# Kernel tuning notes

Hardware: AMD Instinct MI355X
Metric: run time of the kernel (lower is better)

The kernel has to match this reference:

```python
import jax, jax.numpy as jnp
import numpy as np
from jax import lax

DN = ('NCHW', 'OIHW', 'NCHW')

def _conv(x, w, b):
    y = lax.conv_general_dilated(x, w, (1, 1), 'SAME', dimension_numbers=DN)
    return y + b[None, :, None, None]

def setup_inputs() -> dict:
    key = jax.random.key(0)
    ks = jax.random.split(key, 11)
    B, C, H, W = 8, 16, 64, 64
    hid, K = 128, 8192
    s = 0.02
    return {
        'x': jax.random.normal(ks[0], (B, C, H, W), jnp.float32),
        # encoder: Conv2d(C->hid,3x3), GELU, Conv2d(hid->hid,3x3), GELU
        'ew1': jax.random.normal(ks[1], (hid, C, 3, 3), jnp.float32) * s,
        'eb1': jnp.zeros((hid,), jnp.float32),
        'ew2': jax.random.normal(ks[2], (hid, hid, 3, 3), jnp.float32) * s,
        'eb2': jnp.zeros((hid,), jnp.float32),
        # codebook: Embedding(K, hid), init normal std=0.02
        'embed': jax.random.normal(ks[3], (K, hid), jnp.float32) * s,
        # decoder: Conv2d(hid->hid,3x3), GELU, Conv2d(hid->C,1x1), sigmoid
        'dw1': jax.random.normal(ks[4], (hid, hid, 3, 3), jnp.float32) * s,
        'db1': jnp.zeros((hid,), jnp.float32),
        'dw2': jax.random.normal(ks[5], (C, hid, 1, 1), jnp.float32) * s,
        'db2': jnp.zeros((C,), jnp.float32),
    }

def reference(x, ew1, eb1, ew2, eb2, embed, dw1, db1, dw2, db2):
    # --- encoder ---
    h = jax.nn.gelu(_conv(x, ew1, eb1), approximate=False)
    h = jax.nn.gelu(_conv(h, ew2, eb2), approximate=False)  # [B, D, H, W]
    B, D, H, W = h.shape
    flat = jnp.transpose(h, (0, 2, 3, 1)).reshape(B * H * W, D)  # [N, D]
    # --- VQ: pairwise sq-dist + argmin (no_grad in original) ---
    flat_ng = lax.stop_gradient(flat)
    d2 = (jnp.sum(flat_ng * flat_ng, axis=1, keepdims=True)
          - 2.0 * flat_ng @ embed.T
          + jnp.sum(embed * embed, axis=1)[None, :])  # [N, K]
    idx = jnp.argmin(d2, axis=1)  # [N]
    z = idx.reshape(B, H, W)
    q = embed[idx].reshape(B, H, W, D)  # gather
    # --- decoder ---
    qc = jnp.transpose(q, (0, 3, 1, 2))  # NCHW
    y = jax.nn.gelu(_conv(qc, dw1, db1), approximate=False)
    x_hat = jax.nn.sigmoid(_conv(y, dw2, db2))  # [B, C, H, W]
    return x_hat
```

## Files before the change

### kernel.cpp

```cpp
#include <hip/hip_runtime.h>

constexpr int B_ = 8, H_ = 64, W_ = 64, C0 = 16, D_ = 128, K_ = 8192;
constexpr int N_ = B_ * H_ * W_;

typedef __attribute__((ext_vector_type(8))) short short8;
typedef __attribute__((ext_vector_type(4))) float f32x4;

__device__ __forceinline__ float gelu_f(float x) {
    return 0.5f * x * (1.0f + erff(x * 0.70710678118654752440f));
}

__device__ __forceinline__ unsigned short f2bf(float f) {
    unsigned u = __float_as_uint(f);
    u += 0x7fffu + ((u >> 16) & 1u);
    return (unsigned short)(u >> 16);
}

__device__ __forceinline__ void gload_lds16(const void* g, void* l) {
    __builtin_amdgcn_global_load_lds(
        (const __attribute__((address_space(1))) unsigned int*)g,
        (__attribute__((address_space(3))) unsigned int*)l, 16, 0, 0);
}

__global__ __launch_bounds__(256) void prep_kernel(
    const float* __restrict__ x, const float* __restrict__ ew1,
    const float* __restrict__ ew2, const float* __restrict__ dw1,
    const float* __restrict__ embed, unsigned short* __restrict__ xtbf,
    unsigned short* __restrict__ wtbf2, unsigned short* __restrict__ wtbf3,
    float* __restrict__ e2n, unsigned short* __restrict__ embbf,
    unsigned short* __restrict__ wtb1b,
    unsigned long long* __restrict__ partial,
    unsigned short* __restrict__ embq) {
    __shared__ float xt[16][66];
    int blk = blockIdx.x;
    int tid = threadIdx.x;
    if (blk < 512) {
        int b = blk >> 6, h = blk & 63;
        int c = tid >> 4, w4 = tid & 15;
        float4 v = ((const float4*)x)[(b * 16 + c) * 1024 + h * 16 + w4];
        xt[c][w4 * 4 + 0] = v.x;
        xt[c][w4 * 4 + 1] = v.y;
        xt[c][w4 * 4 + 2] = v.z;
        xt[c][w4 * 4 + 3] = v.w;
        __syncthreads();
        int w = tid >> 2, cg = (tid & 3) * 4;
        ushort4 o;
        o.x = f2bf(xt[cg + 0][w]);
        o.y = f2bf(xt[cg + 1][w]);
        o.z = f2bf(xt[cg + 2][w]);
        o.w = f2bf(xt[cg + 3][w]);
        *(ushort4*)(xtbf + (((b * 64 + h) * 64 + w) << 4) + cg) = o;
    } else if (blk < 1664) {
        const float* src = (blk < 1088) ? ew2 : dw1;
        unsigned short* dst = (blk < 1088) ? wtbf2 : wtbf3;
        int i = (blk - ((blk < 1088) ? 512 : 1088)) * 256 + tid;
        int ci = i & 127, co = (i >> 7) & 127, t = i >> 14;
        dst[i] = f2bf(src[(co * 128 + ci) * 9 + t]);
    } else if (blk < 1696) {
        int k = (blk - 1664) * 256 + tid;
        const float4* e4 = (const float4*)(embed + (size_t)k * 128);
        float s = 0.0f;
#pragma unroll 8
        for (int i = 0; i < 32; ++i) {
            float4 v = e4[i];
            s += v.x * v.x + v.y * v.y + v.z * v.z + v.w * v.w;
        }
        e2n[k] = -0.5f * s;
    } else if (blk < 2720) {
        int i = (blk - 1696) * 256 + tid;
        float4 v = ((const float4*)embed)[i];
        uint2 o;
        o.x = (unsigned)f2bf(v.x) | ((unsigned)f2bf(v.y) << 16);
        o.y = (unsigned)f2bf(v.z) | ((unsigned)f2bf(v.w) << 16);
        ((uint2*)embbf)[i] = o;
    } else if (blk < 2800) {
        int i = (blk - 2720) * 256 + tid;
        int co = i / 160, kk = i % 160;
        float v = 0.0f;
        if (kk < 144) {
            int t = kk >> 4, ci = kk & 15;
            v = ew1[(co * 16 + ci) * 9 + t];
        }
        wtb1b[i] = f2bf(v);
    } else if (blk < 2928) {
        int i = (blk - 2800) * 256 + tid;
        partial[i] = 0ULL;
    } else {
        int s = (blk - 2928) * 256 + tid;
        int T = s >> 10;
        int rem = s & 1023;
        int kk = rem >> 8, nsp = (rem >> 6) & 3, q = (rem >> 4) & 3,
            r = rem & 15;
        int code = T * 64 + nsp * 16 + r;
        int d0 = kk * 32 + q * 8;
        const float* ep = embed + (size_t)code * 128 + d0;
        unsigned short* op = embq + (size_t)s * 8;
#pragma unroll
        for (int e = 0; e < 8; ++e) op[e] = f2bf(ep[e]);
    }
}

__global__ __launch_bounds__(256, 2) void conv1_mfma_kernel(
    const unsigned short* __restrict__ xtbf,
    const unsigned short* __restrict__ wtb1b,
    const float* __restrict__ bias,
    unsigned short* __restrict__ out) {
    constexpr int LDA = 168;
    __shared__ __align__(16) unsigned short As[64 * LDA];
    int tid = threadIdx.x;
    int wv = tid >> 6, lane = tid & 63;
    int r = lane & 15, q = lane >> 4;
    int h0 = blockIdx.x & 63, b = blockIdx.x >> 6;

    short8 bf1[5][2];
#pragma unroll
    for (int k = 0; k < 5; ++k)
#pragma unroll
        for (int ns = 0; ns < 2; ++ns)
            bf1[k][ns] = *(const short8*)(wtb1b + (wv * 32 + ns * 16 + r) * 160 +
                                          k * 32 + q * 8);

#pragma unroll
    for (int j = 0; j < 5; ++j) {
        int s = tid + j * 256;
        if (s < 1152) {
            int px = s / 18, rem = s % 18;
            int t = rem >> 1, half = rem & 1;
            int hh = h0 + t / 3 - 1, ww = px + t % 3 - 1;
            float4 v = make_float4(0.f, 0.f, 0.f, 0.f);
            if ((unsigned)hh < 64u && (unsigned)ww < 64u)
                v = *(const float4*)(xtbf + (((b * 64 + hh) * 64 + ww) << 4) +
                                     half * 8);
            *(float4*)(As + px * LDA + t * 16 + half * 8) = v;
        } else {
            int z = s - 1152;
            int px = z >> 1, half = z & 1;
            *(float4*)(As + px * LDA + 144 + half * 8) =
                make_float4(0.f, 0.f, 0.f, 0.f);
        }
    }
    __syncthreads();

    f32x4 acc[4][2];
#pragma unroll
    for (int ms = 0; ms < 4; ++ms)
#pragma unroll
        for (int ns = 0; ns < 2; ++ns) acc[ms][ns] = (f32x4){0.f, 0.f, 0.f, 0.f};

#pragma unroll
    for (int k = 0; k < 5; ++k) {
        short8 af[4];
#pragma unroll
        for (int ms = 0; ms < 4; ++ms)
            af[ms] = *(const short8*)(As + (ms * 16 + r) * LDA + k * 32 + q * 8);
#pragma unroll
        for (int ms = 0; ms < 4; ++ms)
#pragma unroll
            for (int ns = 0; ns < 2; ++ns)
                acc[ms][ns] = __builtin_amdgcn_mfma_f32_16x16x32_bf16(
                    af[ms], bf1[k][ns], acc[ms][ns], 0, 0, 0);
    }

#pragma unroll
    for (int ns = 0; ns < 2; ++ns) {
        int co = wv * 32 + ns * 16 + r;
        float bv = bias[co];
#pragma unroll
        for (int ms = 0; ms < 4; ++ms)
#pragma unroll
            for (int rg = 0; rg < 4; ++rg) {
                int px = ms * 16 + q * 4 + rg;
                int pix = (b * 64 + h0) * 64 + px;
                out[(size_t)pix * 128 + co] = f2bf(gelu_f(acc[ms][ns][rg] + bv));
            }
    }
}

template <bool OUT_BF16, bool GATHER, bool FUSE>
__global__ __launch_bounds__(256, 2) void conv3x3_mfma_kernel(
    const unsigned short* __restrict__ in,
    const unsigned long long* __restrict__ gidx,
    const unsigned short* __restrict__ wtb,
    const float* __restrict__ bias,
    const float* __restrict__ w2,
    const float* __restrict__ b2,
    void* __restrict__ out_) {
    constexpr int LDC = 136;
    __shared__ __align__(16) unsigned short As[3 * 66 * LDC];
    __shared__ __align__(16) float ws2[FUSE ? 2048 : 4];
    int tid = threadIdx.x;
    int wv = tid >> 6, lane = tid & 63;
    int r = lane & 15, q = lane >> 4;
    int h0 = blockIdx.x & 63, b = blockIdx.x >> 6;

    constexpr int NJ = FUSE ? 15 : 13;
    for (int j = 0; j < NJ; ++j) {
        int s = tid + j * 256;
        if (s < 3168) {
            int col = s >> 4, chunk = s & 15;
            int ry = col / 66, cx = col % 66;
            int hh = h0 - 1 + ry, ww = cx - 1;
            float4 v = make_float4(0.f, 0.f, 0.f, 0.f);
            if ((unsigned)hh < 64u && (unsigned)ww < 64u) {
                int pix = (b * 64 + hh) * 64 + ww;
                const unsigned short* src;
                if (GATHER) {
                    int k = 8191 - (int)(unsigned)(gidx[pix] & 0xFFFFFFFFu);
                    src = in + (size_t)k * 128;
                } else {
                    src = in + (size_t)pix * 128;
                }
                v = *(const float4*)(src + chunk * 8);
            }
            *(float4*)(As + col * LDC + chunk * 8) = v;
        } else if (FUSE && s < 3680) {
            int i = s - 3168;
            ((float4*)ws2)[i] = ((const float4*)w2)[i];
        }
    }
    __syncthreads();

    f32x4 acc[4][2];
#pragma unroll
    for (int ms = 0; ms < 4; ++ms)
#pragma unroll
        for (int ns = 0; ns < 2; ++ns) acc[ms][ns] = (f32x4){0.f, 0.f, 0.f, 0.f};

    const unsigned short* wbase = wtb + (wv * 32 + r) * 128 + q * 8;
    short8 bfp[2][2];
    bfp[0][0] = *(const short8*)(wbase);
    bfp[0][1] = *(const short8*)(wbase + 2048);
    int gcur = 0;
    for (int t = 0; t < 9; ++t) {
        int dy = t / 3, dx = t % 3;
#pragma unroll
        for (int k = 0; k < 4; ++k) {
            int cur = gcur & 1, nxt = cur ^ 1;
            if (gcur < 35) {
                int g1 = gcur + 1;
                int t1 = g1 >> 2, k1 = g1 & 3;
                const unsigned short* wp = wbase + t1 * 16384 + k1 * 32;
                bfp[nxt][0] = *(const short8*)(wp);
                bfp[nxt][1] = *(const short8*)(wp + 2048);
            }
            short8 af[4];
#pragma unroll
            for (int ms = 0; ms < 4; ++ms) {
                int col = dy * 66 + ms * 16 + r + dx;
                af[ms] = *(const short8*)(As + col * LDC + k * 32 + q * 8);
            }
#pragma unroll
            for (int ms = 0; ms < 4; ++ms)
#pragma unroll
                for (int ns = 0; ns < 2; ++ns)
                    acc[ms][ns] = __builtin_amdgcn_mfma_f32_16x16x32_bf16(
                        af[ms], bfp[cur][ns], acc[ms][ns], 0, 0, 0);
            ++gcur;
        }
    }

    if (!FUSE) {
#pragma unroll
        for (int ns = 0; ns < 2; ++ns) {
            int co = wv * 32 + ns * 16 + r;
            float bv = bias[co];
#pragma unroll
            for (int ms = 0; ms < 4; ++ms)
#pragma unroll
                for (int rg = 0; rg < 4; ++rg) {
                    int px = ms * 16 + q * 4 + rg;
                    int pix = (b * 64 + h0) * 64 + px;
                    float g = gelu_f(acc[ms][ns][rg] + bv);
                    if (OUT_BF16)
                        ((unsigned short*)out_)[(size_t)pix * 128 + co] = f2bf(g);
                    else
                        ((float*)out_)[(size_t)pix * 128 + co] = g;
                }
        }
    } else {
        __syncthreads();
        float* gbuf = (float*)As;
#pragma unroll
        for (int ns = 0; ns < 2; ++ns) {
            int co = wv * 32 + ns * 16 + r;
            float bv = bias[co];
#pragma unroll
            for (int ms = 0; ms < 4; ++ms)
#pragma unroll
                for (int rg = 0; rg < 4; ++rg) {
                    int px = ms * 16 + q * 4 + rg;
                    gbuf[px * 132 + co] = gelu_f(acc[ms][ns][rg] + bv);
                }
        }
        __syncthreads();
        int w_ = tid & 63, c0 = (tid >> 6) * 4;
        float a4[4] = {b2[c0], b2[c0 + 1], b2[c0 + 2], b2[c0 + 3]};
#pragma unroll 4
        for (int ci = 0; ci < 128; ci += 4) {
            float4 yv = *(const float4*)&gbuf[w_ * 132 + ci];
#pragma unroll
            for (int jc = 0; jc < 4; ++jc) {
                float4 wv4 = *(const float4*)&ws2[(c0 + jc) * 128 + ci];
                a4[jc] += yv.x * wv4.x + yv.y * wv4.y + yv.z * wv4.z +
                          yv.w * wv4.w;
            }
        }
        float* outp = (float*)out_;
#pragma unroll
        for (int jc = 0; jc < 4; ++jc) {
            float v = 1.0f / (1.0f + expf(-a4[jc]));
            outp[(((size_t)b * 16 + c0 + jc) * 64 + h0) * 64 + w_] = v;
        }
    }
}

__global__ __launch_bounds__(256, 2) void vq_mfma_kernel(
    const unsigned short* __restrict__ flatbf,
    const unsigned short* __restrict__ embq,
    const float* __restrict__ e2n,
    unsigned long long* __restrict__ partial) {
    __shared__ __align__(16) unsigned short Bs[2][8192];
    int tid = threadIdx.x;
    int wv = tid >> 6, lane = tid & 63;
    int r = lane & 15, q = lane >> 4;
    int p_h = wv & 1;
    int c_s = wv >> 1;
    int half = blockIdx.x & 1;
    int m0 = (blockIdx.x >> 1) * 64;
    int kbase = half * 4096;
    int t0 = half * 64;

    short8 af[4][2];
#pragma unroll
    for (int kk = 0; kk < 4; ++kk)
#pragma unroll
        for (int ms = 0; ms < 2; ++ms)
            af[kk][ms] = *(const short8*)(
                flatbf + (size_t)(m0 + p_h * 32 + ms * 16 + r) * 128 +
                kk * 32 + q * 8);

    const float* e2p = e2n + kbase + c_s * 32 + r;
    float e2a = e2p[0], e2b = e2p[16];
    float e2nx0 = 0.f, e2nx1 = 0.f;

    {
        const unsigned short* src = embq + (size_t)t0 * 8192;
#pragma unroll
        for (int j = 0; j < 4; ++j) {
            int o = (j * 4 + wv) * 512;
            gload_lds16(src + o + lane * 8, &Bs[0][o]);
        }
    }

    float best[2][4];
#pragma unroll
    for (int ms = 0; ms < 2; ++ms)
#pragma unroll
        for (int rg = 0; rg < 4; ++rg) best[ms][rg] = -3.4e38f;

    __syncthreads();

    f32x4 acc[2][2];
#pragma unroll
    for (int ms = 0; ms < 2; ++ms) {
        acc[ms][0] = (f32x4){e2a, e2a, e2a, e2a};
        acc[ms][1] = (f32x4){e2b, e2b, e2b, e2b};
    }

    int cur = 0;
#pragma unroll 1
    for (int it = 0; it < 64; ++it) {
        if (it < 63) {
            const unsigned short* src = embq + (size_t)(t0 + it + 1) * 8192;
            unsigned short* dst = &Bs[cur ^ 1][0];
#pragma unroll
            for (int j = 0; j < 4; ++j) {
                int o = (j * 4 + wv) * 512;
                gload_lds16(src + o + lane * 8, dst + o);
            }
            e2nx0 = e2p[(it + 1) * 64];
            e2nx1 = e2p[(it + 1) * 64 + 16];
        }
        const unsigned short* bb = &Bs[cur][0];
#pragma unroll
        for (int kk = 0; kk < 4; ++kk) {
            short8 bf0 = *(const short8*)(bb + kk * 2048 + (c_s * 2) * 512 +
                                          q * 128 + r * 8);
            short8 bf1 = *(const short8*)(bb + kk * 2048 + (c_s * 2 + 1) * 512 +
                                          q * 128 + r * 8);
#pragma unroll
            for (int ms = 0; ms < 2; ++ms) {
                acc[ms][0] = __builtin_amdgcn_mfma_f32_16x16x32_bf16(
                    af[kk][ms], bf0, acc[ms][0], 0, 0, 0);
                acc[ms][1] = __builtin_amdgcn_mfma_f32_16x16x32_bf16(
                    af[kk][ms], bf1, acc[ms][1], 0, 0, 0);
            }
        }
        unsigned kb = (unsigned)(2047 - ((it & 31) * 64 + c_s * 32 + r));
#pragma unroll
        for (int ms = 0; ms < 2; ++ms)
#pragma unroll
            for (int rg = 0; rg < 4; ++rg) {
                float u0 = __uint_as_float(
                    (__float_as_uint(acc[ms][0][rg]) & 0xFFFFF800u) | kb);
                float u1 = __uint_as_float(
                    (__float_as_uint(acc[ms][1][rg]) & 0xFFFFF800u) |
                    (kb - 16u));
                best[ms][rg] = fmaxf(best[ms][rg], fmaxf(u0, u1));
            }
        if ((it & 31) == 31) {
#pragma unroll
            for (int ms = 0; ms < 2; ++ms)
#pragma unroll
                for (int rg = 0; rg < 4; ++rg) {
                    float v = best[ms][rg];
#pragma unroll
                    for (int m = 1; m < 16; m <<= 1)
                        v = fmaxf(v, __shfl_xor(v, m));
                    if (r == 0) {
                        unsigned bits = __float_as_uint(v);
                        int cand = 2047 - (int)(bits & 2047u);
                        int code = kbase + (it >> 5) * 2048 + cand;
                        unsigned sb = (bits & 0x80000000u) ? ~bits
                                                           : (bits | 0x80000000u);
                        unsigned long long packed =
                            ((unsigned long long)sb << 32) |
                            (unsigned)(8191 - code);
                        atomicMax(
                            partial + m0 + p_h * 32 + ms * 16 + q * 4 + rg,
                            packed);
                    }
                    best[ms][rg] = -3.4e38f;
                }
        }
        if (it < 63) {
#pragma unroll
            for (int ms = 0; ms < 2; ++ms) {
                acc[ms][0] = (f32x4){e2nx0, e2nx0, e2nx0, e2nx0};
                acc[ms][1] = (f32x4){e2nx1, e2nx1, e2nx1, e2nx1};
            }
        }
        __syncthreads();
        cur ^= 1;
    }
}

extern "C" void kernel_launch(void* const* d_in, const int* in_sizes, int n_in,
                              void* d_out, int out_size, void* d_ws,
                              size_t ws_size, hipStream_t stream) {
    const float* x = (const float*)d_in[0];
    const float* ew1 = (const float*)d_in[1];
    const float* eb1 = (const float*)d_in[2];
    const float* ew2 = (const float*)d_in[3];
    const float* eb2 = (const float*)d_in[4];
    const float* embed = (const float*)d_in[5];
    const float* dw1 = (const float*)d_in[6];
    const float* db1 = (const float*)d_in[7];
    const float* dw2 = (const float*)d_in[8];
    const float* db2 = (const float*)d_in[9];
    float* out = (float*)d_out;

    float* e2n = (float*)d_ws;
    unsigned long long* partial =
        (unsigned long long*)(e2n + 8192);
    unsigned short* xtbf = (unsigned short*)(partial + 32768);
    unsigned short* wtb1b = xtbf + 524288;
    unsigned short* wtbf2 = wtb1b + 20480;
    unsigned short* wtbf3 = wtbf2 + 147456;
    unsigned short* embbf = wtbf3 + 147456;
    unsigned short* abf = embbf + 1048576;
    unsigned short* flatbf = abf + 4194304;
    unsigned short* embq = flatbf + 4194304;

    prep_kernel<<<3440, 256, 0, stream>>>(x, ew1, ew2, dw1, embed, xtbf, wtbf2,
                                          wtbf3, e2n, embbf, wtb1b, partial,
                                          embq);
    conv1_mfma_kernel<<<512, 256, 0, stream>>>(xtbf, wtb1b, eb1, abf);
    conv3x3_mfma_kernel<true, false, false><<<512, 256, 0, stream>>>(
        abf, nullptr, wtbf2, eb2, nullptr, nullptr, flatbf);
    vq_mfma_kernel<<<1024, 256, 0, stream>>>(flatbf, embq, e2n, partial);
    conv3x3_mfma_kernel<false, true, true><<<512, 256, 0, stream>>>(
        embbf, partial, wtbf3, db1, dw2, db2, out);
}
```

Baseline: 222.8 us.

## Stage conv weights through double-buffered LDS via async global-to-LDS loads

The 3x3 conv weights are reordered in the prep kernel into per-(tap, k-chunk) 4096-element blocks laid out in MFMA fragment order. The conv kernel now streams each block into a double-buffered LDS area with global_load_lds, instead of loading B fragments straight from global memory into registers. The aim is to hide global weight-load latency behind the MFMA work and make the loads contiguous. In exchange it adds 16 KB of LDS per block and a __syncthreads on every one of the 36 iterations, and it relies on the async LDS writes having completed before each barrier.

```diff
diff --git a/kernel.cpp b/kernel.cpp
--- a/kernel.cpp
+++ b/kernel.cpp
@@ -54,7 +54,10 @@
         const float* src = (blk < 1088) ? ew2 : dw1;
         unsigned short* dst = (blk < 1088) ? wtbf2 : wtbf3;
         int i = (blk - ((blk < 1088) ? 512 : 1088)) * 256 + tid;
-        int ci = i & 127, co = (i >> 7) & 127, t = i >> 14;
+        int g = i >> 12, rem = i & 4095;
+        int ns = rem >> 9, q = (rem >> 7) & 3, r = (rem >> 3) & 15, e = rem & 7;
+        int t = g >> 2, k = g & 3;
+        int co = ns * 16 + r, ci = k * 32 + q * 8 + e;
         dst[i] = f2bf(src[(co * 128 + ci) * 9 + t]);
     } else if (blk < 1696) {
         int k = (blk - 1664) * 256 + tid;
@@ -187,11 +190,16 @@
     void* __restrict__ out_) {
     constexpr int LDC = 136;
     __shared__ __align__(16) unsigned short As[3 * 66 * LDC];
+    __shared__ __align__(16) unsigned short Ws[2][4096];
     __shared__ __align__(16) float ws2[FUSE ? 2048 : 4];
     int tid = threadIdx.x;
     int wv = tid >> 6, lane = tid & 63;
     int r = lane & 15, q = lane >> 4;
     int h0 = blockIdx.x & 63, b = blockIdx.x >> 6;
+
+    gload_lds16(wtb + (wv * 2) * 512 + lane * 8, &Ws[0][(wv * 2) * 512]);
+    gload_lds16(wtb + (wv * 2 + 1) * 512 + lane * 8,
+                &Ws[0][(wv * 2 + 1) * 512]);
 
     constexpr int NJ = FUSE ? 15 : 13;
     for (int j = 0; j < NJ; ++j) {
@@ -226,37 +234,35 @@
 #pragma unroll
         for (int ns = 0; ns < 2; ++ns) acc[ms][ns] = (f32x4){0.f, 0.f, 0.f, 0.f};
 
-    const unsigned short* wbase = wtb + (wv * 32 + r) * 128 + q * 8;
-    short8 bfp[2][2];
-    bfp[0][0] = *(const short8*)(wbase);
-    bfp[0][1] = *(const short8*)(wbase + 2048);
-    int gcur = 0;
-    for (int t = 0; t < 9; ++t) {
-        int dy = t / 3, dx = t % 3;
-#pragma unroll
-        for (int k = 0; k < 4; ++k) {
-            int cur = gcur & 1, nxt = cur ^ 1;
-            if (gcur < 35) {
-                int g1 = gcur + 1;
-                int t1 = g1 >> 2, k1 = g1 & 3;
-                const unsigned short* wp = wbase + t1 * 16384 + k1 * 32;
-                bfp[nxt][0] = *(const short8*)(wp);
-                bfp[nxt][1] = *(const short8*)(wp + 2048);
-            }
-            short8 af[4];
-#pragma unroll
-            for (int ms = 0; ms < 4; ++ms) {
-                int col = dy * 66 + ms * 16 + r + dx;
-                af[ms] = *(const short8*)(As + col * LDC + k * 32 + q * 8);
-            }
-#pragma unroll
-            for (int ms = 0; ms < 4; ++ms)
-#pragma unroll
-                for (int ns = 0; ns < 2; ++ns)
-                    acc[ms][ns] = __builtin_amdgcn_mfma_f32_16x16x32_bf16(
-                        af[ms], bfp[cur][ns], acc[ms][ns], 0, 0, 0);
-            ++gcur;
-        }
+    int cur = 0;
+#pragma unroll 4
+    for (int g = 0; g < 36; ++g) {
+        if (g < 35) {
+            const unsigned short* wsrc = wtb + (size_t)(g + 1) * 4096;
+            unsigned short* dst = &Ws[cur ^ 1][0];
+            gload_lds16(wsrc + (wv * 2) * 512 + lane * 8, dst + (wv * 2) * 512);
+            gload_lds16(wsrc + (wv * 2 + 1) * 512 + lane * 8,
+                        dst + (wv * 2 + 1) * 512);
+        }
+        int t = g >> 2, k = g & 3;
+        int dy = t / 3, dx = t - dy * 3;
+        short8 bf0 = *(const short8*)(&Ws[cur][(wv * 2) * 512] + lane * 8);
+        short8 bf1 = *(const short8*)(&Ws[cur][(wv * 2 + 1) * 512] + lane * 8);
+        short8 af[4];
+#pragma unroll
+        for (int ms = 0; ms < 4; ++ms) {
+            int col = dy * 66 + ms * 16 + r + dx;
+            af[ms] = *(const short8*)(As + col * LDC + k * 32 + q * 8);
+        }
+#pragma unroll
+        for (int ms = 0; ms < 4; ++ms) {
+            acc[ms][0] = __builtin_amdgcn_mfma_f32_16x16x32_bf16(
+                af[ms], bf0, acc[ms][0], 0, 0, 0);
+            acc[ms][1] = __builtin_amdgcn_mfma_f32_16x16x32_bf16(
+                af[ms], bf1, acc[ms][1], 0, 0, 0);
+        }
+        __syncthreads();
+        cur ^= 1;
     }
 
     if (!FUSE) {
```

Result: faster. 211.0 us (median of 2 runs) (-5.3%).
